# Performance work log

Measured on AMD Instinct MI355X. Metric: run time of the kernel, lower is better.

The kernel has to match this reference:

```python
import jax, jax.numpy as jnp
import numpy as np
from jax import lax

B, N, D = 2, 2048, 1024
H = 16
DH = D // H
EXP = 4
INNER = EXP * D
KS = 3
POWER = 2
LN_EPS = 1e-5


def _layer_norm(x, g, b):
    mu = jnp.mean(x, axis=-1, keepdims=True)
    var = jnp.mean(jnp.square(x - mu), axis=-1, keepdims=True)
    return (x - mu) * lax.rsqrt(var + LN_EPS) * g + b


def setup_inputs() -> dict:
    key = jax.random.key(0)
    ks = jax.random.split(key, 12)
    s = 1.0 / np.sqrt(D)
    si = 1.0 / np.sqrt(INNER)
    return {
        "Q_in": jax.random.normal(ks[0], (B, N, D), jnp.float32),
        "X": jax.random.normal(ks[1], (B, N, D), jnp.float32),
        "Wq": jax.random.normal(ks[2], (D, D), jnp.float32) * s,
        "Wk": jax.random.normal(ks[3], (D, D), jnp.float32) * s,
        "Wv": jax.random.normal(ks[4], (D, D), jnp.float32) * s,
        "Wo": jax.random.normal(ks[5], (D, D), jnp.float32) * s,
        "Wup": jax.random.normal(ks[6], (D, 2 * INNER), jnp.float32) * s,
        "conv_w": jax.random.normal(ks[7], (INNER, 1, KS), jnp.float32) * 0.5,
        "Wdown": jax.random.normal(ks[8], (INNER, D), jnp.float32) * si,
        "g1": jnp.ones((D,), jnp.float32),
        "b1": jnp.zeros((D,), jnp.float32),
        "g2": jnp.ones((D,), jnp.float32),
        "b2": jnp.zeros((D,), jnp.float32),
        "dt": jnp.float32(0.1),
    }


def reference(Q_in, X, Wq, Wk, Wv, Wo, Wup, conv_w, Wdown, g1, b1, g2, b2, dt):
    Bn, Nn, d = Q_in.shape
    # --- attention path: kernelized quadratic attention (relu^power) ---
    Hc = _layer_norm(Q_in, g1, b1) + X                     # [B,N,d]
    def heads(x):
        return x.reshape(Bn, Nn, H, DH).transpose(0, 2, 1, 3)  # [B,H,N,dh]
    Qp = heads(Hc @ Wq)
    Kp = heads(Hc @ Wk)
    Vp = heads(Hc @ Wv)
    PhiQ = jax.nn.elu(Qp) + 1.0
    PhiK = jax.nn.elu(Kp) + 1.0
    W = jnp.einsum("bhnd,bhmd->bhnm", PhiQ, PhiK)          # [B,H,N,N]
    W = jnp.maximum(W, 0.0) ** POWER
    Attr = jnp.einsum("bhnm,bhmd->bhnd", W, Vp)
    Norm = jnp.sum(W, axis=-1, keepdims=True) + 1.0
    m = Attr / Norm - Vp                                   # [B,H,N,dh]
    m_concat = m.transpose(0, 2, 1, 3).reshape(Bn, Nn, d)
    dt_safe = jax.nn.softplus(dt)
    Q_interact = Q_in + dt_safe * (m_concat @ Wo)
    # --- gated depthwise-conv FFN (ConvSwiGLU) ---
    Qn2 = _layer_norm(Q_interact, g2, b2)
    GU = Qn2 @ Wup                                         # [B,N,2*INNER]
    G, U = GU[..., :INNER], GU[..., INNER:]
    Hf = jax.nn.silu(G) * U                                # [B,N,INNER]
    Hf_t = Hf.transpose(0, 2, 1)                           # [B,INNER,N]
    pad = (KS - 1) // 2
    Hc_t = lax.conv_general_dilated(
        Hf_t, conv_w, window_strides=(1,), padding=[(pad, pad)],
        dimension_numbers=("NCH", "OIH", "NCH"), feature_group_count=INNER)
    H_out = Hc_t.transpose(0, 2, 1) @ Wdown
    return Q_interact + H_out
```

## Files before the change

### kernel.cpp

```cpp
#include <hip/hip_runtime.h>

typedef unsigned short u16;
typedef __attribute__((ext_vector_type(8))) __bf16 bf16x8;
typedef __attribute__((ext_vector_type(4))) float f32x4;
typedef __attribute__((ext_vector_type(8))) unsigned short us8v;

__device__ __forceinline__ u16 f2bf(float x){
  union { float f; unsigned u; } v; v.f = x;
  unsigned r = v.u + 0x7fffu + ((v.u >> 16) & 1u);
  return (u16)(r >> 16);
}
__device__ __forceinline__ float bf2f(u16 h){
  union { unsigned u; float f; } v; v.u = ((unsigned)h) << 16;
  return v.f;
}
__device__ __forceinline__ void gld16(const void* g, void* l){
  __builtin_amdgcn_global_load_lds((const __attribute__((address_space(1))) unsigned int*)g,
                                   (__attribute__((address_space(3))) unsigned int*)l, 16, 0, 0);
}

__global__ __launch_bounds__(256) void tr_cvt(const float* __restrict__ S, u16* __restrict__ D,
                                              int R, int C){
  __shared__ float t[32][33];
  int c0 = blockIdx.x*32, r0 = blockIdx.y*32;
  int tx = threadIdx.x, ty = threadIdx.y;
  #pragma unroll
  for (int j=0;j<32;j+=8) t[ty+j][tx] = S[(size_t)(r0+ty+j)*C + (c0+tx)];
  __syncthreads();
  #pragma unroll
  for (int j=0;j<32;j+=8) D[(size_t)(c0+ty+j)*R + (r0+tx)] = f2bf(t[tx][ty+j]);
}

__global__ __launch_bounds__(256) void tr_cvt_up(const float* __restrict__ S, u16* __restrict__ D){
  __shared__ float t[32][33];
  int c0 = blockIdx.x*32, r0 = blockIdx.y*32;
  int tx = threadIdx.x, ty = threadIdx.y;
  #pragma unroll
  for (int j=0;j<32;j+=8) t[ty+j][tx] = S[(size_t)(r0+ty+j)*8192 + (c0+tx)];
  __syncthreads();
  #pragma unroll
  for (int j=0;j<32;j+=8){
    int c = c0 + ty + j;
    int rdst = (c < 4096) ? ((c>>4)*32 + (c&15)) : (((c-4096)>>4)*32 + 16 + (c&15));
    D[(size_t)rdst*1024 + (r0+tx)] = f2bf(t[tx][ty+j]);
  }
}

__global__ __launch_bounds__(256) void ln_kernel(const float* __restrict__ Q, const float* __restrict__ X,
    const float* __restrict__ g, const float* __restrict__ b, u16* __restrict__ O){
  int row = blockIdx.x, tid = threadIdx.x;
  const float4 x = ((const float4*)(Q + (size_t)row*1024))[tid];
  float s = x.x + x.y + x.z + x.w;
  float sq = x.x*x.x + x.y*x.y + x.z*x.z + x.w*x.w;
  #pragma unroll
  for (int o=32;o>0;o>>=1){ s += __shfl_xor(s, o); sq += __shfl_xor(sq, o); }
  __shared__ float ss[4], ssq[4];
  int wid = tid>>6;
  if ((tid&63)==0){ ss[wid]=s; ssq[wid]=sq; }
  __syncthreads();
  s = ss[0]+ss[1]+ss[2]+ss[3]; sq = ssq[0]+ssq[1]+ssq[2]+ssq[3];
  float mu = s*(1.0f/1024.0f);
  float var = sq*(1.0f/1024.0f) - mu*mu;
  float rstd = rsqrtf(var + 1e-5f);
  float4 xx = make_float4(0.f,0.f,0.f,0.f);
  if (X) xx = ((const float4*)(X + (size_t)row*1024))[tid];
  float4 gv = ((const float4*)g)[tid];
  float4 bv = ((const float4*)b)[tid];
  ushort4 o;
  o.x = f2bf((x.x-mu)*rstd*gv.x + bv.x + xx.x);
  o.y = f2bf((x.y-mu)*rstd*gv.y + bv.y + xx.y);
  o.z = f2bf((x.z-mu)*rstd*gv.z + bv.z + xx.z);
  o.w = f2bf((x.w-mu)*rstd*gv.w + bv.w + xx.w);
  ((ushort4*)(O + (size_t)row*1024))[tid] = o;
}

__global__ __launch_bounds__(256) void ln2_kernel(const float* __restrict__ P,
    const float* __restrict__ Qin, const float* __restrict__ dtp,
    const float* __restrict__ g, const float* __restrict__ b,
    float* __restrict__ Qint, u16* __restrict__ Qn2){
  int row = blockIdx.x, tid = threadIdx.x;
  float sp = log1pf(__expf(dtp[0]));
  size_t off = (size_t)row*1024;
  float4 p0 = ((const float4*)(P + off))[tid];
  float4 p1 = ((const float4*)(P + 4194304 + off))[tid];
  float4 q  = ((const float4*)(Qin + off))[tid];
  float4 x;
  x.x = q.x + sp*(p0.x+p1.x); x.y = q.y + sp*(p0.y+p1.y);
  x.z = q.z + sp*(p0.z+p1.z); x.w = q.w + sp*(p0.w+p1.w);
  ((float4*)(Qint + off))[tid] = x;
  float s = x.x + x.y + x.z + x.w;
  float sq = x.x*x.x + x.y*x.y + x.z*x.z + x.w*x.w;
  #pragma unroll
  for (int o=32;o>0;o>>=1){ s += __shfl_xor(s, o); sq += __shfl_xor(sq, o); }
  __shared__ float ss[4], ssq[4];
  int wid = tid>>6;
  if ((tid&63)==0){ ss[wid]=s; ssq[wid]=sq; }
  __syncthreads();
  s = ss[0]+ss[1]+ss[2]+ss[3]; sq = ssq[0]+ssq[1]+ssq[2]+ssq[3];
  float mu = s*(1.0f/1024.0f);
  float var = sq*(1.0f/1024.0f) - mu*mu;
  float rstd = rsqrtf(var + 1e-5f);
  float4 gv = ((const float4*)g)[tid];
  float4 bv = ((const float4*)b)[tid];
  ushort4 o;
  o.x = f2bf((x.x-mu)*rstd*gv.x + bv.x);
  o.y = f2bf((x.y-mu)*rstd*gv.y + bv.y);
  o.z = f2bf((x.z-mu)*rstd*gv.z + bv.z);
  o.w = f2bf((x.w-mu)*rstd*gv.w + bv.w);
  ((ushort4*)(Qn2 + off))[tid] = o;
}

template<int EPI>
__global__ __launch_bounds__(256, 3) void gemm_bt(
    const u16* __restrict__ A, const u16* __restrict__ Bt,
    int M, int Nc, int K,
    void* __restrict__ Op, const float* __restrict__ aux, const float* __restrict__ dtp)
{
  __shared__ u16 As[128*32];
  __shared__ u16 Bs[128*32];
  const int tid = threadIdx.x, wid = tid>>6, lane = tid&63;
  const int g = lane>>4, l = lane&15;
  const int row0 = blockIdx.x*128, col0 = blockIdx.y*128;
  const int wr = (wid&1)*64, wc = (wid>>1)*64;
  const int l3 = l & 3;
  f32x4 acc[4][4] = {};
  for (int k0 = 0; k0 < K; k0 += 32){
    __syncthreads();
    #pragma unroll
    for (int i=0;i<2;i++){
      int ch0 = i*256 + wid*64;
      int ch = ch0 + lane;
      int r = ch >> 2, c = ch & 3;
      int cs = c ^ (r & 3);
      gld16(A  + (size_t)(row0+r)*K + k0 + cs*8, (char*)As + ch0*16);
      gld16(Bt + (size_t)(col0+r)*K + k0 + cs*8, (char*)Bs + ch0*16);
    }
    __syncthreads();
    bf16x8 a[4], b[4];
    #pragma unroll
    for (int i=0;i<4;i++) a[i] = *(const bf16x8*)(As + (wr + i*16 + l)*32 + (g^l3)*8);
    #pragma unroll
    for (int j=0;j<4;j++) b[j] = *(const bf16x8*)(Bs + (wc + j*16 + l)*32 + (g^l3)*8);
    #pragma unroll
    for (int i=0;i<4;i++)
      #pragma unroll
      for (int j=0;j<4;j++)
        acc[i][j] = __builtin_amdgcn_mfma_f32_16x16x32_bf16(a[i], b[j], acc[i][j], 0, 0, 0);
  }
  #pragma unroll
  for (int i=0;i<4;i++)
   #pragma unroll
   for (int j=0;j<4;j++)
    #pragma unroll
    for (int r=0;r<4;r++){
      int row = row0 + wr + i*16 + g*4 + r;
      int col = col0 + wc + j*16 + l;
      float v = acc[i][j][r];
      int qk = col >> 10, c = col & 1023;
      int bb = row >> 11, n = row & 2047, h = c >> 6, d = c & 63;
      u16* P = (u16*)Op;
      if (qk == 2){
        P[(size_t)8388608 + (((size_t)(bb*16 + h))*64 + d)*2048 + n] = f2bf(v);
      } else {
        float phi = v > 0.f ? v + 1.f : __expf(v);
        P[(size_t)qk*4194304 + (((size_t)(bb*16 + h))*2048 + n)*64 + d] = f2bf(phi);
      }
    }
}

__global__ __launch_bounds__(256, 2) void gemm_wide_up(
    const u16* __restrict__ A, const u16* __restrict__ Bt, u16* __restrict__ Op)
{
  __shared__ u16 As[256*32];
  __shared__ u16 Bs[128*32];
  const int tid = threadIdx.x, wid = tid>>6, lane = tid&63;
  const int g = lane>>4, l = lane&15, l3 = l&3;
  const int bid = blockIdx.x;
  const int bx = bid & 15;
  const int by = (bid>>7)*8 + ((bid>>4) & 7);
  const int row0 = bx*256, col0 = by*128;
  const int wr = (wid&1)*128, wc = (wid>>1)*64;
  f32x4 acc[8][4] = {};
  for (int k0 = 0; k0 < 1024; k0 += 32){
    __syncthreads();
    #pragma unroll
    for (int i=0;i<4;i++){
      int ch0 = i*256 + wid*64;
      int ch = ch0 + lane;
      int r = ch >> 2, c = ch & 3;
      int cs = c ^ (r & 3);
      gld16(A + (size_t)(row0+r)*1024 + k0 + cs*8, (char*)As + ch0*16);
    }
    #pragma unroll
    for (int i=0;i<2;i++){
      int ch0 = i*256 + wid*64;
      int ch = ch0 + lane;
      int r = ch >> 2, c = ch & 3;
      int cs = c ^ (r & 3);
      gld16(Bt + (size_t)(col0+r)*1024 + k0 + cs*8, (char*)Bs + ch0*16);
    }
    __syncthreads();
    bf16x8 a[8], b[4];
    #pragma unroll
    for (int i=0;i<8;i++) a[i] = *(const bf16x8*)(As + (wr + i*16 + l)*32 + (g^l3)*8);
    #pragma unroll
    for (int j=0;j<4;j++) b[j] = *(const bf16x8*)(Bs + (wc + j*16 + l)*32 + (g^l3)*8);
    #pragma unroll
    for (int i=0;i<8;i++)
      #pragma unroll
      for (int j=0;j<4;j++)
        acc[i][j] = __builtin_amdgcn_mfma_f32_16x16x32_bf16(a[i], b[j], acc[i][j], 0, 0, 0);
  }
  #pragma unroll
  for (int i=0;i<8;i++)
   #pragma unroll
   for (int jj=0;jj<4;jj+=2)
    #pragma unroll
    for (int r=0;r<4;r++){
      int row = row0 + wr + i*16 + g*4 + r;
      int pair = (col0 + wc + jj*16) >> 5;
      float G = acc[i][jj][r], U = acc[i][jj+1][r];
      float hf = G/(1.f+__expf(-G))*U;
      Op[(size_t)row*4096 + pair*16 + l] = f2bf(hf);
    }
}

__global__ __launch_bounds__(256, 3) void gemm_part(
    const u16* __restrict__ A, const u16* __restrict__ Bt,
    int Nc, int K, int Ks, float* __restrict__ Op)
{
  __shared__ u16 As[128*32];
  __shared__ u16 Bs[128*32];
  const int tid = threadIdx.x, wid = tid>>6, lane = tid&63;
  const int g = lane>>4, l = lane&15;
  const int row0 = blockIdx.x*128, col0 = blockIdx.y*128;
  const int kbase = blockIdx.z*Ks;
  const int wr = (wid&1)*64, wc = (wid>>1)*64;
  const int l3 = l & 3;
  f32x4 acc[4][4] = {};
  for (int k0 = kbase; k0 < kbase + Ks; k0 += 32){
    __syncthreads();
    #pragma unroll
    for (int i=0;i<2;i++){
      int ch0 = i*256 + wid*64;
      int ch = ch0 + lane;
      int r = ch >> 2, c = ch & 3;
      int cs = c ^ (r & 3);
      gld16(A  + (size_t)(row0+r)*K + k0 + cs*8, (char*)As + ch0*16);
      gld16(Bt + (size_t)(col0+r)*K + k0 + cs*8, (char*)Bs + ch0*16);
    }
    __syncthreads();
    bf16x8 a[4], b[4];
    #pragma unroll
    for (int i=0;i<4;i++) a[i] = *(const bf16x8*)(As + (wr + i*16 + l)*32 + (g^l3)*8);
    #pragma unroll
    for (int j=0;j<4;j++) b[j] = *(const bf16x8*)(Bs + (wc + j*16 + l)*32 + (g^l3)*8);
    #pragma unroll
    for (int i=0;i<4;i++)
      #pragma unroll
      for (int j=0;j<4;j++)
        acc[i][j] = __builtin_amdgcn_mfma_f32_16x16x32_bf16(a[i], b[j], acc[i][j], 0, 0, 0);
  }
  float* P = Op + (size_t)blockIdx.z*4194304;
  #pragma unroll
  for (int i=0;i<4;i++)
   #pragma unroll
   for (int j=0;j<4;j++)
    #pragma unroll
    for (int r=0;r<4;r++){
      int row = row0 + wr + i*16 + g*4 + r;
      int col = col0 + wc + j*16 + l;
      P[(size_t)row*Nc + col] = acc[i][j][r];
    }
}

__global__ __launch_bounds__(256) void reduce_out(const float* __restrict__ Qint,
    const float* __restrict__ P, float* __restrict__ out){
  size_t i = (size_t)blockIdx.x*256 + threadIdx.x;
  float4 a  = ((const float4*)Qint)[i];
  float4 p0 = ((const float4*)P)[i];
  float4 p1 = ((const float4*)(P + 4194304))[i];
  float4 o;
  o.x = a.x + p0.x + p1.x; o.y = a.y + p0.y + p1.y;
  o.z = a.z + p0.z + p1.z; o.w = a.w + p0.w + p1.w;
  ((float4*)out)[i] = o;
}

__global__ __launch_bounds__(256, 2) void attn_kernel(
    const u16* __restrict__ PhiQ, const u16* __restrict__ PhiK,
    const u16* __restrict__ Vt, u16* __restrict__ Mb)
{
  __shared__ u16 sQ[2][128][32];
  __shared__ u16 sK[2][128][32];
  __shared__ u16 sV[4][64][32];
  __shared__ u16 sW[128*128];
  const int tid = threadIdx.x, wid = tid>>6, lane = tid&63;
  const int g = lane>>4, l = lane&15;
  const int l3 = l & 3;
  const int q0 = blockIdx.x*128, bh = blockIdx.y;
  const u16* Q  = PhiQ + (size_t)bh*2048*64;
  const u16* Kb = PhiK + (size_t)bh*2048*64;
  const u16* V  = Vt   + (size_t)bh*64*2048;
  #pragma unroll
  for (int ks=0; ks<2; ks++)
    #pragma unroll
    for (int i=0;i<2;i++){
      int ch0 = i*256 + wid*64;
      int ch = ch0 + lane;
      int r = ch >> 2, q = ch & 3;
      int qs = q ^ (r & 3);
      gld16(Q + (size_t)(q0+r)*64 + ks*32 + qs*8, (char*)&sQ[ks][0][0] + ch0*16);
    }
  f32x4 accO[2][4] = {};
  float rsum[8] = {0.f,0.f,0.f,0.f,0.f,0.f,0.f,0.f};
  for (int m0 = 0; m0 < 2048; m0 += 128){
    __syncthreads();
    #pragma unroll
    for (int ks=0; ks<2; ks++)
      #pragma unroll
      for (int i=0;i<2;i++){
        int ch0 = i*256 + wid*64;
        int ch = ch0 + lane;
        int r = ch >> 2, q = ch & 3;
        int qs = q ^ (r & 3);
        gld16(Kb + (size_t)(m0+r)*64 + ks*32 + qs*8, (char*)&sK[ks][0][0] + ch0*16);
      }
    #pragma unroll
    for (int c=0; c<4; c++){
      int ch0 = wid*64;
      int ch = ch0 + lane;
      int d = ch >> 2, q = ch & 3;
      int qs = q ^ (d & 3);
      gld16(V + (size_t)d*2048 + m0 + c*32 + qs*8, (char*)&sV[c][0][0] + ch0*16);
    }
    __syncthreads();
    f32x4 st[2][8] = {};
    bf16x8 ak[2][2];
    #pragma unroll
    for (int rt=0;rt<2;rt++)
      #pragma unroll
      for (int ks=0;ks<2;ks++)
        ak[rt][ks] = *(const bf16x8*)&sK[ks][wid*32 + rt*16 + l][(g^l3)*8];
    #pragma unroll
    for (int ct=0;ct<8;ct++){
      #pragma unroll
      for (int ks=0;ks<2;ks++){
        bf16x8 bq = *(const bf16x8*)&sQ[ks][ct*16 + l][(g^l3)*8];
        st[0][ct] = __builtin_amdgcn_mfma_f32_16x16x32_bf16(ak[0][ks], bq, st[0][ct], 0,0,0);
        st[1][ct] = __builtin_amdgcn_mfma_f32_16x16x32_bf16(ak[1][ks], bq, st[1][ct], 0,0,0);
      }
    }
    #pragma unroll
    for (int ct=0;ct<8;ct++){
      float part = 0.f;
      #pragma unroll
      for (int rt=0;rt<2;rt++){
        float s0 = fmaxf(st[rt][ct][0], 0.f), s1 = fmaxf(st[rt][ct][1], 0.f);
        float s2 = fmaxf(st[rt][ct][2], 0.f), s3 = fmaxf(st[rt][ct][3], 0.f);
        float w0 = s0*s0, w1 = s1*s1, w2 = s2*s2, w3 = s3*s3;
        part += w0 + w1 + w2 + w3;
        int n = ct*16 + l;
        int mblk = wid*4 + rt*2 + (g>>1);
        ushort4 w4;
        w4.x = f2bf(w0); w4.y = f2bf(w1); w4.z = f2bf(w2); w4.w = f2bf(w3);
        *(ushort4*)(sW + n*128 + ((mblk ^ l)*8) + (g&1)*4) = w4;
      }
      rsum[ct] += part;
    }
    __syncthreads();
    #pragma unroll
    for (int ks=0;ks<4;ks++){
      int n0 = wid*32 + l, n1 = wid*32 + 16 + l;
      bf16x8 aw0 = *(const bf16x8*)(sW + n0*128 + (((ks*4+g) ^ (n0&15))*8));
      bf16x8 aw1 = *(const bf16x8*)(sW + n1*128 + (((ks*4+g) ^ (n1&15))*8));
      #pragma unroll
      for (int ct=0;ct<4;ct++){
        bf16x8 bv = *(const bf16x8*)&sV[ks][ct*16 + l][(g^l3)*8];
        accO[0][ct] = __builtin_amdgcn_mfma_f32_16x16x32_bf16(aw0, bv, accO[0][ct], 0,0,0);
        accO[1][ct] = __builtin_amdgcn_mfma_f32_16x16x32_bf16(aw1, bv, accO[1][ct], 0,0,0);
      }
    }
  }
  __syncthreads();
  float* sRS = (float*)sW;
  float* sNorm = ((float*)sW) + 512;
  #pragma unroll
  for (int ct=0;ct<8;ct++){
    float v = rsum[ct];
    v += __shfl_xor(v, 16);
    v += __shfl_xor(v, 32);
    rsum[ct] = v;
  }
  if (g == 0){
    #pragma unroll
    for (int ct=0;ct<8;ct++) sRS[wid*128 + ct*16 + l] = rsum[ct];
  }
  __syncthreads();
  if (tid < 128) sNorm[tid] = sRS[tid] + sRS[128+tid] + sRS[256+tid] + sRS[384+tid] + 1.0f;
  __syncthreads();
  const int bb = bh >> 4, h = bh & 15;
  #pragma unroll
  for (int rt=0;rt<2;rt++)
   #pragma unroll
   for (int ct=0;ct<4;ct++)
    #pragma unroll
    for (int r=0;r<4;r++){
      int n = wid*32 + rt*16 + g*4 + r;
      int d = ct*16 + l;
      float norm = sNorm[n];
      float vv = bf2f(V[(size_t)d*2048 + q0 + n]);
      float mv = accO[rt][ct][r]/norm - vv;
      Mb[((size_t)(bb*2048) + q0 + n)*1024 + h*64 + d] = f2bf(mv);
    }
}

__global__ __launch_bounds__(256) void conv_kernel(const u16* __restrict__ Hf, const float* __restrict__ w,
                                                   u16* __restrict__ Cv){
  int row = blockIdx.y;
  int n = row & 2047;
  int c0 = (blockIdx.x*256 + threadIdx.x)*8;
  us8v h0 = {0,0,0,0,0,0,0,0}, h2 = {0,0,0,0,0,0,0,0};
  us8v h1 = *(const us8v*)(Hf + (size_t)row*4096 + c0);
  if (n > 0)    h0 = *(const us8v*)(Hf + (size_t)(row-1)*4096 + c0);
  if (n < 2047) h2 = *(const us8v*)(Hf + (size_t)(row+1)*4096 + c0);
  us8v o;
  #pragma unroll
  for (int e=0;e<8;e++){
    int c = c0 + e;
    float acc = bf2f(h0[e])*w[c*3+0] + bf2f(h1[e])*w[c*3+1] + bf2f(h2[e])*w[c*3+2];
    o[e] = f2bf(acc);
  }
  *(us8v*)(Cv + (size_t)row*4096 + c0) = o;
}

extern "C" void kernel_launch(void* const* d_in, const int* in_sizes, int n_in,
                              void* d_out, int out_size, void* d_ws, size_t ws_size,
                              hipStream_t stream)
{
  const float* Q_in  = (const float*)d_in[0];
  const float* X     = (const float*)d_in[1];
  const float* Wq    = (const float*)d_in[2];
  const float* Wk    = (const float*)d_in[3];
  const float* Wv    = (const float*)d_in[4];
  const float* Wo    = (const float*)d_in[5];
  const float* Wup   = (const float*)d_in[6];
  const float* convw = (const float*)d_in[7];
  const float* Wdown = (const float*)d_in[8];
  const float* g1    = (const float*)d_in[9];
  const float* b1    = (const float*)d_in[10];
  const float* g2    = (const float*)d_in[11];
  const float* b2    = (const float*)d_in[12];
  const float* dt    = (const float*)d_in[13];
  float* out = (float*)d_out;

  char* ws = (char*)d_ws;
  const size_t MB = (size_t)1 << 20;
  u16* HcB   = (u16*)(ws + 0*MB);
  u16* WqkvT = (u16*)(ws + 8*MB);
  u16* WoT   = (u16*)(ws + 14*MB);
  u16* PhiQ  = (u16*)(ws + 16*MB);
  u16* Vt    = (u16*)(ws + 32*MB);
  u16* Mb    = (u16*)(ws + 40*MB);
  float* Po  = (float*)(ws + 48*MB);
  u16* WupT  = (u16*)(ws + 80*MB);
  u16* WdT   = (u16*)(ws + 96*MB);
  float* Qint = (float*)(ws + 104*MB);
  u16* Qn2   = (u16*)(ws + 120*MB);
  u16* Hf    = (u16*)(ws + 0*MB);
  u16* Cv    = (u16*)(ws + 40*MB);
  float* Pd  = (float*)(ws + 0*MB);
  u16* PhiK  = PhiQ + 4194304;

  dim3 tb(32, 8);
  tr_cvt<<<dim3(32, 32),  tb, 0, stream>>>(Wq,    WqkvT,               1024, 1024);
  tr_cvt<<<dim3(32, 32),  tb, 0, stream>>>(Wk,    WqkvT + 1024*1024,   1024, 1024);
  tr_cvt<<<dim3(32, 32),  tb, 0, stream>>>(Wv,    WqkvT + 2*1024*1024, 1024, 1024);
  tr_cvt<<<dim3(32, 32),  tb, 0, stream>>>(Wo,    WoT, 1024, 1024);
  tr_cvt_up<<<dim3(256, 32), tb, 0, stream>>>(Wup, WupT);
  tr_cvt<<<dim3(32, 128), tb, 0, stream>>>(Wdown, WdT, 4096, 1024);

  ln_kernel<<<4096, 256, 0, stream>>>(Q_in, X, g1, b1, HcB);

  gemm_bt<5><<<dim3(32, 24), 256, 0, stream>>>(HcB, WqkvT, 4096, 3072, 1024, PhiQ, nullptr, nullptr);

  attn_kernel<<<dim3(16, 32), 256, 0, stream>>>(PhiQ, PhiK, Vt, Mb);

  gemm_part<<<dim3(32, 8, 2), 256, 0, stream>>>(Mb, WoT, 1024, 1024, 512, Po);

  ln2_kernel<<<4096, 256, 0, stream>>>(Po, Q_in, dt, g2, b2, Qint, Qn2);

  gemm_wide_up<<<1024, 256, 0, stream>>>(Qn2, WupT, Hf);

  conv_kernel<<<dim3(2, 4096), 256, 0, stream>>>(Hf, convw, Cv);

  gemm_part<<<dim3(32, 8, 2), 256, 0, stream>>>(Cv, WdT, 1024, 4096, 2048, Pd);
  reduce_out<<<4096, 256, 0, stream>>>(Qint, Pd, out);
}
```

Baseline: 451.6 us.

## Merge weight transposes into one launch, vectorize V stores, keep Q in registers

New measurement: 434.4 us. 1.04x faster.

```diff
diff --git a/kernel.cpp b/kernel.cpp
--- a/kernel.cpp
+++ b/kernel.cpp
@@ -19,30 +19,46 @@
                                    (__attribute__((address_space(3))) unsigned int*)l, 16, 0, 0);
 }
 
-__global__ __launch_bounds__(256) void tr_cvt(const float* __restrict__ S, u16* __restrict__ D,
-                                              int R, int C){
+__global__ __launch_bounds__(256) void tr_all(
+    const float* __restrict__ Wq, const float* __restrict__ Wk,
+    const float* __restrict__ Wv, const float* __restrict__ Wo,
+    const float* __restrict__ Wup, const float* __restrict__ Wdown,
+    u16* __restrict__ WqkvT, u16* __restrict__ WoT,
+    u16* __restrict__ WupT, u16* __restrict__ WdT)
+{
   __shared__ float t[32][33];
-  int c0 = blockIdx.x*32, r0 = blockIdx.y*32;
   int tx = threadIdx.x, ty = threadIdx.y;
-  #pragma unroll
-  for (int j=0;j<32;j+=8) t[ty+j][tx] = S[(size_t)(r0+ty+j)*C + (c0+tx)];
-  __syncthreads();
-  #pragma unroll
-  for (int j=0;j<32;j+=8) D[(size_t)(c0+ty+j)*R + (r0+tx)] = f2bf(t[tx][ty+j]);
-}
-
-__global__ __launch_bounds__(256) void tr_cvt_up(const float* __restrict__ S, u16* __restrict__ D){
-  __shared__ float t[32][33];
-  int c0 = blockIdx.x*32, r0 = blockIdx.y*32;
-  int tx = threadIdx.x, ty = threadIdx.y;
-  #pragma unroll
-  for (int j=0;j<32;j+=8) t[ty+j][tx] = S[(size_t)(r0+ty+j)*8192 + (c0+tx)];
-  __syncthreads();
-  #pragma unroll
-  for (int j=0;j<32;j+=8){
-    int c = c0 + ty + j;
-    int rdst = (c < 4096) ? ((c>>4)*32 + (c&15)) : (((c-4096)>>4)*32 + 16 + (c&15));
-    D[(size_t)rdst*1024 + (r0+tx)] = f2bf(t[tx][ty+j]);
+  int id = blockIdx.x;
+  if (id < 4096){
+    int w = id >> 10, b = id & 1023;
+    int c0 = (b & 31)*32, r0 = (b >> 5)*32;
+    const float* S = (w==0)?Wq:(w==1)?Wk:(w==2)?Wv:Wo;
+    u16* D = (w==3)? WoT : (WqkvT + (size_t)w*1024*1024);
+    #pragma unroll
+    for (int j=0;j<32;j+=8) t[ty+j][tx] = S[(size_t)(r0+ty+j)*1024 + (c0+tx)];
+    __syncthreads();
+    #pragma unroll
+    for (int j=0;j<32;j+=8) D[(size_t)(c0+ty+j)*1024 + (r0+tx)] = f2bf(t[tx][ty+j]);
+  } else if (id < 12288){
+    int b = id - 4096;
+    int c0 = (b & 255)*32, r0 = (b >> 8)*32;
+    #pragma unroll
+    for (int j=0;j<32;j+=8) t[ty+j][tx] = Wup[(size_t)(r0+ty+j)*8192 + (c0+tx)];
+    __syncthreads();
+    #pragma unroll
+    for (int j=0;j<32;j+=8){
+      int c = c0 + ty + j;
+      int rdst = (c < 4096) ? ((c>>4)*32 + (c&15)) : (((c-4096)>>4)*32 + 16 + (c&15));
+      WupT[(size_t)rdst*1024 + (r0+tx)] = f2bf(t[tx][ty+j]);
+    }
+  } else {
+    int b = id - 12288;
+    int c0 = (b & 31)*32, r0 = (b >> 5)*32;
+    #pragma unroll
+    for (int j=0;j<32;j+=8) t[ty+j][tx] = Wdown[(size_t)(r0+ty+j)*1024 + (c0+tx)];
+    __syncthreads();
+    #pragma unroll
+    for (int j=0;j<32;j+=8) WdT[(size_t)(c0+ty+j)*4096 + (r0+tx)] = f2bf(t[tx][ty+j]);
   }
 }
 
@@ -110,11 +126,8 @@
   ((ushort4*)(Qn2 + off))[tid] = o;
 }
 
-template<int EPI>
-__global__ __launch_bounds__(256, 3) void gemm_bt(
-    const u16* __restrict__ A, const u16* __restrict__ Bt,
-    int M, int Nc, int K,
-    void* __restrict__ Op, const float* __restrict__ aux, const float* __restrict__ dtp)
+__global__ __launch_bounds__(256, 3) void gemm_qkv(
+    const u16* __restrict__ A, const u16* __restrict__ Bt, void* __restrict__ Op)
 {
   __shared__ u16 As[128*32];
   __shared__ u16 Bs[128*32];
@@ -124,7 +137,7 @@
   const int wr = (wid&1)*64, wc = (wid>>1)*64;
   const int l3 = l & 3;
   f32x4 acc[4][4] = {};
-  for (int k0 = 0; k0 < K; k0 += 32){
+  for (int k0 = 0; k0 < 1024; k0 += 32){
     __syncthreads();
     #pragma unroll
     for (int i=0;i<2;i++){
@@ -132,8 +145,8 @@
       int ch = ch0 + lane;
       int r = ch >> 2, c = ch & 3;
       int cs = c ^ (r & 3);
-      gld16(A  + (size_t)(row0+r)*K + k0 + cs*8, (char*)As + ch0*16);
-      gld16(Bt + (size_t)(col0+r)*K + k0 + cs*8, (char*)Bs + ch0*16);
+      gld16(A  + (size_t)(row0+r)*1024 + k0 + cs*8, (char*)As + ch0*16);
+      gld16(Bt + (size_t)(col0+r)*1024 + k0 + cs*8, (char*)Bs + ch0*16);
     }
     __syncthreads();
     bf16x8 a[4], b[4];
@@ -147,25 +160,30 @@
       for (int j=0;j<4;j++)
         acc[i][j] = __builtin_amdgcn_mfma_f32_16x16x32_bf16(a[i], b[j], acc[i][j], 0, 0, 0);
   }
+  u16* P = (u16*)Op;
   #pragma unroll
   for (int i=0;i<4;i++)
    #pragma unroll
-   for (int j=0;j<4;j++)
-    #pragma unroll
-    for (int r=0;r<4;r++){
-      int row = row0 + wr + i*16 + g*4 + r;
-      int col = col0 + wc + j*16 + l;
-      float v = acc[i][j][r];
-      int qk = col >> 10, c = col & 1023;
-      int bb = row >> 11, n = row & 2047, h = c >> 6, d = c & 63;
-      u16* P = (u16*)Op;
-      if (qk == 2){
-        P[(size_t)8388608 + (((size_t)(bb*16 + h))*64 + d)*2048 + n] = f2bf(v);
-      } else {
-        float phi = v > 0.f ? v + 1.f : __expf(v);
-        P[(size_t)qk*4194304 + (((size_t)(bb*16 + h))*2048 + n)*64 + d] = f2bf(phi);
-      }
-    }
+   for (int j=0;j<4;j++){
+     int col = col0 + wc + j*16 + l;
+     int qk = col >> 10, c = col & 1023;
+     int h = c >> 6, d = c & 63;
+     int rowb = row0 + wr + i*16 + g*4;
+     int bb = rowb >> 11, n = rowb & 2047;
+     if (qk == 2){
+       ushort4 vs;
+       vs.x = f2bf(acc[i][j][0]); vs.y = f2bf(acc[i][j][1]);
+       vs.z = f2bf(acc[i][j][2]); vs.w = f2bf(acc[i][j][3]);
+       *(ushort4*)(P + (size_t)8388608 + (((size_t)(bb*16 + h))*64 + d)*2048 + n) = vs;
+     } else {
+       #pragma unroll
+       for (int r=0;r<4;r++){
+         float v = acc[i][j][r];
+         float phi = v > 0.f ? v + 1.f : __expf(v);
+         P[(size_t)qk*4194304 + (((size_t)(bb*16 + h))*2048 + (n+r))*64 + d] = f2bf(phi);
+       }
+     }
+   }
 }
 
 __global__ __launch_bounds__(256, 2) void gemm_wide_up(
@@ -290,7 +308,6 @@
     const u16* __restrict__ PhiQ, const u16* __restrict__ PhiK,
     const u16* __restrict__ Vt, u16* __restrict__ Mb)
 {
-  __shared__ u16 sQ[2][128][32];
   __shared__ u16 sK[2][128][32];
   __shared__ u16 sV[4][64][32];
   __shared__ u16 sW[128*128];
@@ -301,16 +318,12 @@
   const u16* Q  = PhiQ + (size_t)bh*2048*64;
   const u16* Kb = PhiK + (size_t)bh*2048*64;
   const u16* V  = Vt   + (size_t)bh*64*2048;
-  #pragma unroll
-  for (int ks=0; ks<2; ks++)
-    #pragma unroll
-    for (int i=0;i<2;i++){
-      int ch0 = i*256 + wid*64;
-      int ch = ch0 + lane;
-      int r = ch >> 2, q = ch & 3;
-      int qs = q ^ (r & 3);
-      gld16(Q + (size_t)(q0+r)*64 + ks*32 + qs*8, (char*)&sQ[ks][0][0] + ch0*16);
-    }
+  bf16x8 bq[8][2];
+  #pragma unroll
+  for (int ct=0;ct<8;ct++)
+    #pragma unroll
+    for (int ks=0;ks<2;ks++)
+      bq[ct][ks] = *(const bf16x8*)(Q + (size_t)(q0 + ct*16 + l)*64 + ks*32 + g*8);
   f32x4 accO[2][4] = {};
   float rsum[8] = {0.f,0.f,0.f,0.f,0.f,0.f,0.f,0.f};
   for (int m0 = 0; m0 < 2048; m0 += 128){
@@ -345,9 +358,8 @@
     for (int ct=0;ct<8;ct++){
       #pragma unroll
       for (int ks=0;ks<2;ks++){
-        bf16x8 bq = *(const bf16x8*)&sQ[ks][ct*16 + l][(g^l3)*8];
-        st[0][ct] = __builtin_amdgcn_mfma_f32_16x16x32_bf16(ak[0][ks], bq, st[0][ct], 0,0,0);
-        st[1][ct] = __builtin_amdgcn_mfma_f32_16x16x32_bf16(ak[1][ks], bq, st[1][ct], 0,0,0);
+        st[0][ct] = __builtin_amdgcn_mfma_f32_16x16x32_bf16(ak[0][ks], bq[ct][ks], st[0][ct], 0,0,0);
+        st[1][ct] = __builtin_amdgcn_mfma_f32_16x16x32_bf16(ak[1][ks], bq[ct][ks], st[1][ct], 0,0,0);
       }
     }
     #pragma unroll
@@ -471,17 +483,12 @@
   float* Pd  = (float*)(ws + 0*MB);
   u16* PhiK  = PhiQ + 4194304;
 
-  dim3 tb(32, 8);
-  tr_cvt<<<dim3(32, 32),  tb, 0, stream>>>(Wq,    WqkvT,               1024, 1024);
-  tr_cvt<<<dim3(32, 32),  tb, 0, stream>>>(Wk,    WqkvT + 1024*1024,   1024, 1024);
-  tr_cvt<<<dim3(32, 32),  tb, 0, stream>>>(Wv,    WqkvT + 2*1024*1024, 1024, 1024);
-  tr_cvt<<<dim3(32, 32),  tb, 0, stream>>>(Wo,    WoT, 1024, 1024);
-  tr_cvt_up<<<dim3(256, 32), tb, 0, stream>>>(Wup, WupT);
-  tr_cvt<<<dim3(32, 128), tb, 0, stream>>>(Wdown, WdT, 4096, 1024);
+  tr_all<<<16384, dim3(32, 8), 0, stream>>>(Wq, Wk, Wv, Wo, Wup, Wdown,
+                                            WqkvT, WoT, WupT, WdT);
 
   ln_kernel<<<4096, 256, 0, stream>>>(Q_in, X, g1, b1, HcB);
 
-  gemm_bt<5><<<dim3(32, 24), 256, 0, stream>>>(HcB, WqkvT, 4096, 3072, 1024, PhiQ, nullptr, nullptr);
+  gemm_qkv<<<dim3(32, 24), 256, 0, stream>>>(HcB, WqkvT, PhiQ);
 
   attn_kernel<<<dim3(16, 32), 256, 0, stream>>>(PhiQ, PhiK, Vt, Mb);
 
```
